# Optimization experiments

Hardware: AMD Instinct MI355X
Metric: run time of the kernel (lower is better)

Reference implementation:

```python
import jax, jax.numpy as jnp
import numpy as np

B, NQ, NKV = 2, 1024, 4096
DQ = 1024          # query_dim == context_dim
H, DH = 16, 64     # heads, dim_head
INNER = H * DH     # 1024
SCALE = DH ** -0.5


def setup_inputs() -> dict:
    key = jax.random.key(0)
    ks = jax.random.split(key, 6)
    s = 1.0 / np.sqrt(DQ)
    return {
        "x": jax.random.normal(ks[0], (B, NQ, DQ), dtype=jnp.float32),
        "context": jax.random.normal(ks[1], (B, NKV, DQ), dtype=jnp.float32),
        "Wq": jax.random.normal(ks[2], (DQ, INNER), dtype=jnp.float32) * s,
        "Wkv": jax.random.normal(ks[3], (DQ, 2 * INNER), dtype=jnp.float32) * s,
        "Wout": jax.random.normal(ks[4], (INNER, DQ), dtype=jnp.float32) * (1.0 / np.sqrt(INNER)),
        "b_out": jax.random.normal(ks[5], (DQ,), dtype=jnp.float32) * 0.01,
    }


def _split_heads(t):
    # b n (h d) -> b h n d
    b, n, _ = t.shape
    return t.reshape(b, n, H, DH).transpose(0, 2, 1, 3)


def reference(x, context, Wq, Wkv, Wout, b_out):
    q = x @ Wq                       # [B, NQ, INNER]
    kv = context @ Wkv               # [B, NKV, 2*INNER]
    k, v = jnp.split(kv, 2, axis=-1)
    q, k, v = map(_split_heads, (q, k, v))          # [B, H, n, DH]
    sim = jnp.einsum("bhid,bhjd->bhij", q, k) * SCALE  # [B, H, NQ, NKV]
    attn = jax.nn.softmax(sim, axis=-1)
    out = jnp.einsum("bhij,bhjd->bhid", attn, v)       # [B, H, NQ, DH]
    out = out.transpose(0, 2, 1, 3).reshape(B, NQ, INNER)  # (b h) n d -> b n (h d)
    return out @ Wout + b_out
```

## Files before the change

### kernel.cpp

```cpp
#include <hip/hip_runtime.h>
#include <stdint.h>

#define B_    2
#define NQ_   1024
#define NKV_  4096
#define DQ_   1024
#define H_    16
#define DH_   64
#define INNER_ 1024

typedef unsigned short u16;
typedef uint32_t u32;
typedef __bf16 bf16x8 __attribute__((ext_vector_type(8)));
typedef float  f32x4  __attribute__((ext_vector_type(4)));

__device__ __forceinline__ u16 f2bf(float x) {
  union { float f; uint32_t u; } v; v.f = x;
  uint32_t r = v.u + 0x7FFFu + ((v.u >> 16) & 1u);
  return (u16)(r >> 16);
}
__device__ __forceinline__ u32 pack2(float a, float b) {
  return (u32)f2bf(a) | ((u32)f2bf(b) << 16);
}
__device__ __forceinline__ u32 pack2rn(float a, float b) {
  union { float f; u32 u; } x, y; x.f = a; y.f = b;
  return __builtin_amdgcn_perm(y.u + 0x8000u, x.u + 0x8000u, 0x07060302u);
}
__device__ __forceinline__ float bf2f(u16 s) {
  union { float f; uint32_t u; } v; v.u = ((uint32_t)s) << 16; return v.f;
}

__device__ __forceinline__ void gload16(const void* g, void* l) {
  __builtin_amdgcn_global_load_lds((const __attribute__((address_space(1))) void*)g,
                                   (__attribute__((address_space(3))) void*)l,
                                   16, 0, 0);
}

__global__ __launch_bounds__(256) void prep(const float* __restrict__ x,
                                            const float* __restrict__ ctx,
                                            const float* __restrict__ Wq,
                                            const float* __restrict__ Wkv,
                                            const float* __restrict__ Wout,
                                            u16* __restrict__ xb,
                                            u16* __restrict__ ctxb,
                                            u16* __restrict__ WqT,
                                            u16* __restrict__ WkvT,
                                            u16* __restrict__ WoutT) {
  int bid = blockIdx.x;
  if (bid < 1280) {
    const float* src; u16* dst; int fbase;
    if (bid < 256) { src = x;   dst = xb;   fbase = bid * 2048; }
    else           { src = ctx; dst = ctxb; fbase = (bid - 256) * 2048; }
#pragma unroll
    for (int u = 0; u < 8; ++u) {
      int i = (fbase + u * 256 + threadIdx.x) * 4;
      float4 v = *(const float4*)(src + i);
      uint2 o; o.x = pack2(v.x, v.y); o.y = pack2(v.z, v.w);
      *(uint2*)(dst + i) = o;
    }
    return;
  }
  __shared__ float tile[32][33];
  const float* W; u16* Wt; int K, N, local, nsh;
  int b2 = bid - 1280;
  if (b2 < 1024)      { W = Wq;   Wt = WqT;   K = 1024; N = 1024; local = b2;        nsh = 5; }
  else if (b2 < 3072) { W = Wkv;  Wt = WkvT;  K = 1024; N = 2048; local = b2 - 1024; nsh = 6; }
  else                { W = Wout; Wt = WoutT; K = 1024; N = 1024; local = b2 - 3072; nsh = 5; }
  int n0 = (local & ((1 << nsh) - 1)) * 32;
  int k0 = (local >> nsh) * 32;
  int tx = threadIdx.x & 31, ty = threadIdx.x >> 5;
  for (int i = ty; i < 32; i += 8)
    tile[i][tx] = W[(size_t)(k0 + i) * N + n0 + tx];
  __syncthreads();
  for (int i = ty; i < 32; i += 8)
    Wt[(size_t)(n0 + i) * K + k0 + tx] = f2bf(tile[tx][i]);
}

__global__ __launch_bounds__(512, 2) void kv_gemm(const u16* __restrict__ ctxb,
                                                  const u16* __restrict__ WkvT,
                                                  u16* __restrict__ kb,
                                                  u16* __restrict__ vTb) {
  __shared__ __align__(16) u16 As[2][256 * 64];
  __shared__ __align__(16) u16 Bs[2][256 * 64];
  const int tid = threadIdx.x;
  const int lane = tid & 63;
  const int w = tid >> 6;
  const int wr = w >> 2, wc = w & 3;
  const int l15 = lane & 15, quad = lane >> 4;
  const int K = 1024;

  int bid = blockIdx.x;
  int wgid = (bid & 7) * 32 + (bid >> 3);
  const int tm = wgid >> 3, tn = wgid & 7;
  const int m0 = tm * 256, n0 = tn * 256;
  const u16* Ag = ctxb + (size_t)m0 * K;
  const u16* Bg = WkvT + (size_t)n0 * K;

  size_t offA[2][2], offB[2][2];
#pragma unroll
  for (int ah = 0; ah < 2; ++ah)
#pragma unroll
    for (int p = 0; p < 2; ++p) {
      int c = p * 512 + (w << 6) + lane;
      int s = ah * 128 + (c >> 3);
      int col = ((c & 7) ^ (s & 7)) << 3;
      int rA = ((s >> 6) & 1) * 128 + ((s >> 7) & 1) * 64 + (s & 63);
      int rB = ((s >> 5) & 3) * 64 + ((s >> 7) & 1) * 32 + (s & 31);
      offA[ah][p] = (size_t)rA * 1024 + col;
      offB[ah][p] = (size_t)rB * 1024 + col;
    }

#define STAGE_A(bufi, ah, kk) do { \
    gload16(Ag + offA[ah][0] + (kk), &As[bufi][(ah) * 8192 + (w << 9)]); \
    gload16(Ag + offA[ah][1] + (kk), &As[bufi][(ah) * 8192 + 4096 + (w << 9)]); \
  } while (0)
#define STAGE_B(bufi, bh, kk) do { \
    gload16(Bg + offB[bh][0] + (kk), &Bs[bufi][(bh) * 8192 + (w << 9)]); \
    gload16(Bg + offB[bh][1] + (kk), &Bs[bufi][(bh) * 8192 + 4096 + (w << 9)]); \
  } while (0)
#define LDA2(dst, i8, bufi) do { \
    const int _s = ((i8) >> 2) * 128 + wr * 64 + ((i8) & 3) * 16 + l15; \
    const u16* _p = &As[bufi][_s * 64]; const int _x = _s & 7; \
    dst[0] = *(const bf16x8*)&_p[(quad ^ _x) << 3]; \
    dst[1] = *(const bf16x8*)&_p[((quad + 4) ^ _x) << 3]; \
  } while (0)
#define LDB2(dst, j, bufi) do { \
    const int _s = ((j) >> 1) * 128 + wc * 32 + ((j) & 1) * 16 + l15; \
    const u16* _p = &Bs[bufi][_s * 64]; const int _x = _s & 7; \
    dst[0] = *(const bf16x8*)&_p[(quad ^ _x) << 3]; \
    dst[1] = *(const bf16x8*)&_p[((quad + 4) ^ _x) << 3]; \
  } while (0)
#define MF(i0, j0, bb) do { \
    _Pragma("unroll") \
    for (int _i = 0; _i < 4; ++_i) { \
      acc[(i0) + _i][(j0)    ] = __builtin_amdgcn_mfma_f32_16x16x32_bf16(a[_i][0], bb[0][0], acc[(i0) + _i][(j0)    ], 0, 0, 0); \
      acc[(i0) + _i][(j0)    ] = __builtin_amdgcn_mfma_f32_16x16x32_bf16(a[_i][1], bb[0][1], acc[(i0) + _i][(j0)    ], 0, 0, 0); \
      acc[(i0) + _i][(j0) + 1] = __builtin_amdgcn_mfma_f32_16x16x32_bf16(a[_i][0], bb[1][0], acc[(i0) + _i][(j0) + 1], 0, 0, 0); \
      acc[(i0) + _i][(j0) + 1] = __builtin_amdgcn_mfma_f32_16x16x32_bf16(a[_i][1], bb[1][1], acc[(i0) + _i][(j0) + 1], 0, 0, 0); \
    } \
  } while (0)

  f32x4 acc[8][4] = {};
  bf16x8 a[4][2], b[2][2], c2[2][2];

  STAGE_A(0, 0, 0);
  STAGE_B(0, 0, 0);
  STAGE_B(0, 1, 0);
  STAGE_A(0, 1, 0);
  asm volatile("s_waitcnt vmcnt(4)" ::: "memory");
  __builtin_amdgcn_s_barrier();

#define KTILE(cur, nxt, kk, STG, W1, W2) do { \
     \
    LDB2(b[0], 0, cur); LDB2(b[1], 1, cur); \
    LDA2(a[0], 0, cur); LDA2(a[1], 1, cur); LDA2(a[2], 2, cur); LDA2(a[3], 3, cur); \
    if (STG) STAGE_A(nxt, 0, kk); \
    __builtin_amdgcn_s_barrier(); \
    asm volatile("s_waitcnt lgkmcnt(0)" ::: "memory"); \
    __builtin_amdgcn_s_setprio(1); MF(0, 0, b); __builtin_amdgcn_s_setprio(0); \
    asm volatile("s_waitcnt " W1 ::: "memory"); \
    __builtin_amdgcn_s_barrier(); \
     \
    LDB2(c2[0], 2, cur); LDB2(c2[1], 3, cur); \
    if (STG) STAGE_B(nxt, 0, kk); \
    __builtin_amdgcn_s_barrier(); \
    asm volatile("s_waitcnt lgkmcnt(0)" ::: "memory"); \
    __builtin_amdgcn_s_setprio(1); MF(0, 2, c2); __builtin_amdgcn_s_setprio(0); \
    asm volatile("s_waitcnt " W2 ::: "memory"); \
    __builtin_amdgcn_s_barrier(); \
     \
    LDA2(a[0], 4, cur); LDA2(a[1], 5, cur); LDA2(a[2], 6, cur); LDA2(a[3], 7, cur); \
    if (STG) STAGE_B(nxt, 1, kk); \
    __builtin_amdgcn_s_barrier(); \
    asm volatile("s_waitcnt lgkmcnt(0)" ::: "memory"); \
    __builtin_amdgcn_s_setprio(1); MF(4, 0, b); __builtin_amdgcn_s_setprio(0); \
    __builtin_amdgcn_s_barrier(); \
     \
    if (STG) STAGE_A(nxt, 1, kk); \
    __builtin_amdgcn_s_barrier(); \
    __builtin_amdgcn_s_setprio(1); MF(4, 2, c2); __builtin_amdgcn_s_setprio(0); \
    if (STG) { asm volatile("s_waitcnt vmcnt(4)" ::: "memory"); } \
    __builtin_amdgcn_s_barrier(); \
  } while (0)

  for (int T = 0; T < 15; ++T) {
    const int cur = T & 1, nxt = cur ^ 1, kk = (T + 1) * 64;
    KTILE(cur, nxt, kk, 1, "vmcnt(4)", "vmcnt(4)");
  }
  KTILE(1, 0, 0, 0, "vmcnt(2)", "vmcnt(0)");

  if (tn < 4) {
#pragma unroll
    for (int i8 = 0; i8 < 8; ++i8)
#pragma unroll
      for (int j = 0; j < 4; ++j) {
        int col = n0 + wc * 64 + j * 16 + l15;
#pragma unroll
        for (int r = 0; r < 4; ++r) {
          int row = m0 + wr * 128 + i8 * 16 + quad * 4 + r;
          kb[(size_t)row * 1024 + col] = f2bf(acc[i8][j][r]);
        }
      }
  } else {
    const int bb_ = m0 >> 12;
#pragma unroll
    for (int i8 = 0; i8 < 8; ++i8) {
      int kvr = (m0 & 4095) + wr * 128 + i8 * 16 + quad * 4;
#pragma unroll
      for (int j = 0; j < 4; ++j) {
        int c = (n0 - 1024) + wc * 64 + j * 16 + l15;
        int h = c >> 6, dh = c & 63;
        uint2 st;
        st.x = pack2(acc[i8][j][0], acc[i8][j][1]);
        st.y = pack2(acc[i8][j][2], acc[i8][j][3]);
        *(uint2*)&vTb[((size_t)((bb_ * 16 + h) * 64 + dh)) * NKV_ + kvr] = st;
      }
    }
  }
#undef STAGE_A
#undef STAGE_B
#undef LDA2
#undef LDB2
#undef MF
#undef KTILE
}

__global__ __launch_bounds__(256) void q_gemm(const u16* __restrict__ A,
                                              const u16* __restrict__ Bt,
                                              u16* __restrict__ outp) {
  __shared__ __align__(16) u16 As[64 * 32];
  __shared__ __align__(16) u16 Bs[128 * 32];
  const int tid = threadIdx.x;
  const int lane = tid & 63;
  const int w = tid >> 6;
  const int wr = w >> 1, wc = w & 1;
  const int l15 = lane & 15, quad = lane >> 4;
  const int unit = blockIdx.x;
  const int m0 = (unit >> 3) * 64, n0 = (unit & 7) * 128;
  const int K = 1024, N = 1024;

  const u16* Ab = A + (size_t)m0 * K;
  const u16* Bb = Bt + (size_t)n0 * K;
  f32x4 acc[2][4] = {};

  const int ar = tid >> 2, ac = (tid & 3) << 3;
  const int q1 = w * 64 + lane, q2 = q1 + 256;
  const int br1 = q1 >> 2, bc1 = (q1 & 3) << 3;
  const int br2 = q2 >> 2, bc2 = (q2 & 3) << 3;

  for (int k0 = 0; k0 < K; k0 += 32) {
    __syncthreads();
    gload16(Ab + (size_t)ar * K + k0 + ac, &As[w * 512]);
    gload16(Bb + (size_t)br1 * K + k0 + bc1, &Bs[w * 512]);
    gload16(Bb + (size_t)br2 * K + k0 + bc2, &Bs[2048 + w * 512]);
    __syncthreads();
    bf16x8 af[2], bfr[4];
#pragma unroll
    for (int i = 0; i < 2; ++i)
      af[i] = *(const bf16x8*)&As[(wr * 32 + i * 16 + l15) * 32 + quad * 8];
#pragma unroll
    for (int j = 0; j < 4; ++j)
      bfr[j] = *(const bf16x8*)&Bs[(wc * 64 + j * 16 + l15) * 32 + quad * 8];
#pragma unroll
    for (int i = 0; i < 2; ++i)
#pragma unroll
      for (int j = 0; j < 4; ++j)
        acc[i][j] = __builtin_amdgcn_mfma_f32_16x16x32_bf16(af[i], bfr[j], acc[i][j], 0, 0, 0);
  }

#pragma unroll
  for (int i = 0; i < 2; ++i)
#pragma unroll
    for (int j = 0; j < 4; ++j) {
      int col = n0 + wc * 64 + j * 16 + l15;
#pragma unroll
      for (int r = 0; r < 4; ++r) {
        int row = m0 + wr * 32 + i * 16 + quad * 4 + r;
        outp[(size_t)row * N + col] = f2bf(acc[i][j][r]);
      }
    }
}

__global__ __launch_bounds__(256) void out_gemm(const u16* __restrict__ A,
                                                const u16* __restrict__ Bt,
                                                float* __restrict__ Cout,
                                                const float* __restrict__ bias) {
  __shared__ __align__(16) u16 As[64 * 32];
  __shared__ __align__(16) u16 Bs[128 * 32];
  const int tid = threadIdx.x;
  const int lane = tid & 63;
  const int w = tid >> 6;
  const int wr = w >> 1, wc = w & 1;
  const int l15 = lane & 15, quad = lane >> 4;
  const int unit = blockIdx.x;
  const int m0 = (unit >> 3) * 64, n0 = (unit & 7) * 128;
  const int K = 1024, N = 1024;

  const u16* Ab = A + (size_t)m0 * K;
  const u16* Bb = Bt + (size_t)n0 * K;
  f32x4 acc[2][4] = {};

  const int ar = tid >> 2, ac = (tid & 3) << 3;
  const int q1 = w * 64 + lane, q2 = q1 + 256;
  const int br1 = q1 >> 2, bc1 = (q1 & 3) << 3;
  const int br2 = q2 >> 2, bc2 = (q2 & 3) << 3;

  for (int k0 = 0; k0 < K; k0 += 32) {
    __syncthreads();
    gload16(Ab + (size_t)ar * K + k0 + ac, &As[w * 512]);
    gload16(Bb + (size_t)br1 * K + k0 + bc1, &Bs[w * 512]);
    gload16(Bb + (size_t)br2 * K + k0 + bc2, &Bs[2048 + w * 512]);
    __syncthreads();
    bf16x8 af[2], bfr[4];
#pragma unroll
    for (int i = 0; i < 2; ++i)
      af[i] = *(const bf16x8*)&As[(wr * 32 + i * 16 + l15) * 32 + quad * 8];
#pragma unroll
    for (int j = 0; j < 4; ++j)
      bfr[j] = *(const bf16x8*)&Bs[(wc * 64 + j * 16 + l15) * 32 + quad * 8];
#pragma unroll
    for (int i = 0; i < 2; ++i)
#pragma unroll
      for (int j = 0; j < 4; ++j)
        acc[i][j] = __builtin_amdgcn_mfma_f32_16x16x32_bf16(af[i], bfr[j], acc[i][j], 0, 0, 0);
  }

#pragma unroll
  for (int i = 0; i < 2; ++i)
#pragma unroll
    for (int j = 0; j < 4; ++j) {
      int col = n0 + wc * 64 + j * 16 + l15;
      float bv = bias[col];
#pragma unroll
      for (int r = 0; r < 4; ++r) {
        int row = m0 + wr * 32 + i * 16 + quad * 4 + r;
        Cout[(size_t)row * N + col] = acc[i][j][r] + bv;
      }
    }
}

__global__ __launch_bounds__(256, 2) void attn_kernel(const u16* __restrict__ qg,
                                                      const u16* __restrict__ kb,
                                                      const u16* __restrict__ vT,
                                                      u16* __restrict__ attn_out) {
  __shared__ __align__(16) u16 Ks[128 * 64];
  __shared__ __align__(16) u16 Vs[64 * 128];
  __shared__ __align__(16) u32 P32[4 * 4 * 16 * 20];
  __shared__ float Lr[4][4][16];

  const int tid = threadIdx.x;
  const int lane = tid & 63;
  const int w = tid >> 6;
  const int l15 = lane & 15, quad = lane >> 4;
  const int bh = blockIdx.x, b = bh >> 4, h = bh & 15;
  const int q0 = blockIdx.y * 64;

  const float SC = 0.125f * 1.44269504088896340736f;
  union { u16 s[8]; bf16x8 v; } qf[4][2];
#pragma unroll
  for (int t = 0; t < 4; ++t)
#pragma unroll
    for (int kc = 0; kc < 2; ++kc) {
      const u16* qp = qg + (size_t)(b * NQ_ + q0 + t * 16 + l15) * INNER_ + h * 64 +
                      kc * 32 + quad * 8;
      union { u16 s[8]; uint4 u; } tmp;
      tmp.u = *(const uint4*)qp;
#pragma unroll
      for (int e = 0; e < 8; ++e) qf[t][kc].s[e] = f2bf(bf2f(tmp.s[e]) * SC);
    }

#define STAGEKV(j0) do { \
    _Pragma("unroll") \
    for (int i_ = 0; i_ < 4; ++i_) { \
      int s_ = i_ * 256 + tid; \
      int kr = s_ >> 3, kg = (s_ ^ kr) & 7; \
      gload16(kb + (size_t)(b * NKV_ + (j0) + kr) * 1024 + h * 64 + kg * 8, \
              &Ks[(i_ * 256 + w * 64) * 8]); \
      int vr = s_ >> 4, vg = (s_ ^ vr) & 15; \
      gload16(vT + (size_t)(bh * 64 + vr) * NKV_ + (j0) + vg * 8, \
              &Vs[(i_ * 256 + w * 64) * 8]); \
    } \
  } while (0)

  f32x4 Oacc[4][4] = {};
  float l_lane[4] = {0.f, 0.f, 0.f, 0.f};

  STAGEKV(0);

  for (int it = 0; it < 32; ++it) {
    __syncthreads();

    bf16x8 kf[2][2];
#pragma unroll
    for (int kvt = 0; kvt < 2; ++kvt)
#pragma unroll
      for (int kc = 0; kc < 2; ++kc)
        kf[kvt][kc] = *(const bf16x8*)
          &Ks[(w * 32 + kvt * 16 + l15) * 64 + (((kc * 4 + quad) ^ l15) & 7) * 8];
    bf16x8 vf[4];
#pragma unroll
    for (int d = 0; d < 4; ++d)
      vf[d] = *(const bf16x8*)
        &Vs[(d * 16 + l15) * 128 + (((w * 4 + quad) ^ l15) & 15) * 8];

    __syncthreads();

    if (it < 31) STAGEKV((it + 1) * 128);

    f32x4 sacc[2][4] = {};
    __builtin_amdgcn_s_setprio(1);
#pragma unroll
    for (int kvt = 0; kvt < 2; ++kvt)
#pragma unroll
      for (int t = 0; t < 4; ++t)
#pragma unroll
        for (int kc = 0; kc < 2; ++kc)
          sacc[kvt][t] = __builtin_amdgcn_mfma_f32_16x16x32_bf16(
              kf[kvt][kc], qf[t][kc].v, sacc[kvt][t], 0, 0, 0);
    __builtin_amdgcn_s_setprio(0);

#pragma unroll
    for (int kvt = 0; kvt < 2; ++kvt)
#pragma unroll
      for (int t = 0; t < 4; ++t) {
        float p0 = __builtin_amdgcn_exp2f(sacc[kvt][t][0]);
        float p1 = __builtin_amdgcn_exp2f(sacc[kvt][t][1]);
        float p2 = __builtin_amdgcn_exp2f(sacc[kvt][t][2]);
        float p3 = __builtin_amdgcn_exp2f(sacc[kvt][t][3]);
        l_lane[t] += (p0 + p1) + (p2 + p3);
        uint2 pk; pk.x = pack2rn(p0, p1); pk.y = pack2rn(p2, p3);
        *(uint2*)&P32[((w * 4 + t) * 16 + l15) * 20 + kvt * 8 + quad * 2] = pk;
      }

    bf16x8 pf[4];
#pragma unroll
    for (int t = 0; t < 4; ++t)
      pf[t] = *(const bf16x8*)&P32[((w * 4 + t) * 16 + l15) * 20 + quad * 4];
    __builtin_amdgcn_s_setprio(1);
#pragma unroll
    for (int d = 0; d < 4; ++d)
#pragma unroll
      for (int t = 0; t < 4; ++t)
        Oacc[d][t] = __builtin_amdgcn_mfma_f32_16x16x32_bf16(vf[d], pf[t], Oacc[d][t],
                                                             0, 0, 0);
    __builtin_amdgcn_s_setprio(0);
  }
#undef STAGEKV

#pragma unroll
  for (int t = 0; t < 4; ++t) {
    l_lane[t] += __shfl_xor(l_lane[t], 16);
    l_lane[t] += __shfl_xor(l_lane[t], 32);
  }
  if (quad == 0) {
#pragma unroll
    for (int t = 0; t < 4; ++t) Lr[w][t][l15] = l_lane[t];
  }
  __syncthreads();
  float inv = 1.0f / (Lr[0][w][l15] + Lr[1][w][l15] + Lr[2][w][l15] + Lr[3][w][l15]);

  float* red = (float*)P32;
  u16* ob = attn_out + (size_t)(b * NQ_ + q0 + w * 16 + l15) * INNER_ + h * 64;
#pragma unroll
  for (int d = 0; d < 4; ++d) {
    __syncthreads();
#pragma unroll
    for (int t = 0; t < 4; ++t)
      *(f32x4*)&red[(w * 4 + t) * 256 + quad * 64 + l15 * 4] = Oacc[d][t];
    __syncthreads();
    f32x4 r = *(const f32x4*)&red[(0 * 4 + w) * 256 + quad * 64 + l15 * 4];
#pragma unroll
    for (int ww = 1; ww < 4; ++ww) {
      f32x4 c = *(const f32x4*)&red[(ww * 4 + w) * 256 + quad * 64 + l15 * 4];
      r[0] += c[0]; r[1] += c[1]; r[2] += c[2]; r[3] += c[3];
    }
    *(u32*)(ob + d * 16 + quad * 4)     = pack2(r[0] * inv, r[1] * inv);
    *(u32*)(ob + d * 16 + quad * 4 + 2) = pack2(r[2] * inv, r[3] * inv);
  }
}

extern "C" void kernel_launch(void* const* d_in, const int* in_sizes, int n_in,
                              void* d_out, int out_size, void* d_ws, size_t ws_size,
                              hipStream_t stream) {
  const float* x    = (const float*)d_in[0];
  const float* ctx  = (const float*)d_in[1];
  const float* Wq   = (const float*)d_in[2];
  const float* Wkv  = (const float*)d_in[3];
  const float* Wout = (const float*)d_in[4];
  const float* bout = (const float*)d_in[5];

  char* ws = (char*)d_ws;
  u16* xb    = (u16*)(ws + (size_t)( 0u << 20));
  u16* ab    = (u16*)(ws + (size_t)( 0u << 20));
  u16* ctxb  = (u16*)(ws + (size_t)( 4u << 20));
  u16* WqT   = (u16*)(ws + (size_t)(20u << 20));
  u16* WkvT  = (u16*)(ws + (size_t)(22u << 20));
  u16* WoutT = (u16*)(ws + (size_t)(26u << 20));
  u16* qb    = (u16*)(ws + (size_t)(28u << 20));
  u16* kb    = (u16*)(ws + (size_t)(32u << 20));
  u16* vTb   = (u16*)(ws + (size_t)(48u << 20));

  prep<<<5376, 256, 0, stream>>>(x, ctx, Wq, Wkv, Wout, xb, ctxb, WqT, WkvT, WoutT);
  q_gemm<<<256, 256, 0, stream>>>(xb, WqT, qb);
  kv_gemm<<<256, 512, 0, stream>>>(ctxb, WkvT, kb, vTb);
  attn_kernel<<<dim3(32, 16), 256, 0, stream>>>(qb, kb, vTb, ab);
  out_gemm<<<256, 256, 0, stream>>>(ab, WoutT, (float*)d_out, bout);
}
```

Before: 228.5 us.

## Pre-tile K/V into per-wave images, drop block barriers and LDS P round-trip

The KV GEMM epilogue now writes K and V^T in a tiled, pre-swizzled per-(bh, 128-row tile, wave) layout. Each attention wave can then stage its own contiguous 32-key slice into a private double-buffered LDS region with no __syncthreads in the main loop. The softmax probabilities are packed with v_cvt_pk_bf16_f32 and rearranged into the PV MFMA operand layout using permlane32_swap and shuffles, replacing the write-then-read through LDS. This removes block-wide barriers and LDS traffic in the hot loop, at the cost of more cross-lane ops and a more scattered epilogue store pattern in the projection GEMM.

```diff
diff --git a/kernel.cpp b/kernel.cpp
--- a/kernel.cpp
+++ b/kernel.cpp
@@ -22,9 +22,10 @@
 __device__ __forceinline__ u32 pack2(float a, float b) {
   return (u32)f2bf(a) | ((u32)f2bf(b) << 16);
 }
-__device__ __forceinline__ u32 pack2rn(float a, float b) {
-  union { float f; u32 u; } x, y; x.f = a; y.f = b;
-  return __builtin_amdgcn_perm(y.u + 0x8000u, x.u + 0x8000u, 0x07060302u);
+__device__ __forceinline__ u32 cvtpk(float lo, float hi) {
+  u32 r;
+  asm("v_cvt_pk_bf16_f32 %0, %1, %2" : "=v"(r) : "v"(lo), "v"(hi));
+  return r;
 }
 __device__ __forceinline__ float bf2f(u16 s) {
   union { float f; uint32_t u; } v; v.u = ((uint32_t)s) << 16; return v.f;
@@ -151,7 +152,6 @@
   __builtin_amdgcn_s_barrier();
 
 #define KTILE(cur, nxt, kk, STG, W1, W2) do { \
-     \
     LDB2(b[0], 0, cur); LDB2(b[1], 1, cur); \
     LDA2(a[0], 0, cur); LDA2(a[1], 1, cur); LDA2(a[2], 2, cur); LDA2(a[3], 3, cur); \
     if (STG) STAGE_A(nxt, 0, kk); \
@@ -160,7 +160,6 @@
     __builtin_amdgcn_s_setprio(1); MF(0, 0, b); __builtin_amdgcn_s_setprio(0); \
     asm volatile("s_waitcnt " W1 ::: "memory"); \
     __builtin_amdgcn_s_barrier(); \
-     \
     LDB2(c2[0], 2, cur); LDB2(c2[1], 3, cur); \
     if (STG) STAGE_B(nxt, 0, kk); \
     __builtin_amdgcn_s_barrier(); \
@@ -168,14 +167,12 @@
     __builtin_amdgcn_s_setprio(1); MF(0, 2, c2); __builtin_amdgcn_s_setprio(0); \
     asm volatile("s_waitcnt " W2 ::: "memory"); \
     __builtin_amdgcn_s_barrier(); \
-     \
     LDA2(a[0], 4, cur); LDA2(a[1], 5, cur); LDA2(a[2], 6, cur); LDA2(a[3], 7, cur); \
     if (STG) STAGE_B(nxt, 1, kk); \
     __builtin_amdgcn_s_barrier(); \
     asm volatile("s_waitcnt lgkmcnt(0)" ::: "memory"); \
     __builtin_amdgcn_s_setprio(1); MF(4, 0, b); __builtin_amdgcn_s_setprio(0); \
     __builtin_amdgcn_s_barrier(); \
-     \
     if (STG) STAGE_A(nxt, 1, kk); \
     __builtin_amdgcn_s_barrier(); \
     __builtin_amdgcn_s_setprio(1); MF(4, 2, c2); __builtin_amdgcn_s_setprio(0); \
@@ -190,30 +187,38 @@
   KTILE(1, 0, 0, 0, "vmcnt(2)", "vmcnt(0)");
 
   if (tn < 4) {
-#pragma unroll
-    for (int i8 = 0; i8 < 8; ++i8)
+    const int b_ = m0 >> 12;
+    const int h_ = (n0 >> 6) + wc;
+    const int bh_ = b_ * 16 + h_;
+    const int it0 = ((m0 & 4095) >> 7) + wr;
+    const int e = l15 & 7;
+#pragma unroll
+    for (int i8 = 0; i8 < 8; ++i8) {
+      const size_t reg_ = ((size_t)(bh_ * 32 + it0) * 4 + (i8 >> 1)) * 2048;
 #pragma unroll
       for (int j = 0; j < 4; ++j) {
-        int col = n0 + wc * 64 + j * 16 + l15;
+        const int gd = j * 2 + (l15 >> 3);
 #pragma unroll
         for (int r = 0; r < 4; ++r) {
-          int row = m0 + wr * 128 + i8 * 16 + quad * 4 + r;
-          kb[(size_t)row * 1024 + col] = f2bf(acc[i8][j][r]);
+          const int rl = (i8 & 1) * 16 + quad * 4 + r;
+          kb[reg_ + rl * 64 + ((gd ^ rl) & 7) * 8 + e] = f2bf(acc[i8][j][r]);
         }
       }
+    }
   } else {
-    const int bb_ = m0 >> 12;
+    const int b_ = m0 >> 12;
+    const int h_ = ((n0 - 1024) >> 6) + wc;
+    const int bh_ = b_ * 16 + h_;
+    const int it0 = ((m0 & 4095) >> 7) + wr;
 #pragma unroll
     for (int i8 = 0; i8 < 8; ++i8) {
-      int kvr = (m0 & 4095) + wr * 128 + i8 * 16 + quad * 4;
+      const size_t reg_ = ((size_t)(bh_ * 32 + it0) * 4 + (i8 >> 1)) * 2048;
 #pragma unroll
       for (int j = 0; j < 4; ++j) {
-        int c = (n0 - 1024) + wc * 64 + j * 16 + l15;
-        int h = c >> 6, dh = c & 63;
         uint2 st;
         st.x = pack2(acc[i8][j][0], acc[i8][j][1]);
         st.y = pack2(acc[i8][j][2], acc[i8][j][3]);
-        *(uint2*)&vTb[((size_t)((bb_ * 16 + h) * 64 + dh)) * NKV_ + kvr] = st;
+        *(uint2*)&vTb[reg_ + (size_t)(j * 16 + l15) * 32 + (i8 & 1) * 16 + quad * 4] = st;
       }
     }
   }
@@ -339,15 +344,14 @@
     }
 }
 
-__global__ __launch_bounds__(256, 2) void attn_kernel(const u16* __restrict__ qg,
-                                                      const u16* __restrict__ kb,
-                                                      const u16* __restrict__ vT,
+__global__ __launch_bounds__(256, 2) void attn_kernel(const u16* __restrict__ kimg_q,
+                                                      const u16* __restrict__ kimg,
+                                                      const u16* __restrict__ vimg,
                                                       u16* __restrict__ attn_out) {
-  __shared__ __align__(16) u16 Ks[128 * 64];
-  __shared__ __align__(16) u16 Vs[64 * 128];
-  __shared__ __align__(16) u32 P32[4 * 4 * 16 * 20];
+  __shared__ __align__(16) u16 KV[4][2][4096];
   __shared__ float Lr[4][4][16];
 
+  const u16* qg = kimg_q;
   const int tid = threadIdx.x;
   const int lane = tid & 63;
   const int w = tid >> 6;
@@ -369,73 +373,88 @@
       for (int e = 0; e < 8; ++e) qf[t][kc].s[e] = f2bf(bf2f(tmp.s[e]) * SC);
     }
 
-#define STAGEKV(j0) do { \
-    _Pragma("unroll") \
-    for (int i_ = 0; i_ < 4; ++i_) { \
-      int s_ = i_ * 256 + tid; \
-      int kr = s_ >> 3, kg = (s_ ^ kr) & 7; \
-      gload16(kb + (size_t)(b * NKV_ + (j0) + kr) * 1024 + h * 64 + kg * 8, \
-              &Ks[(i_ * 256 + w * 64) * 8]); \
-      int vr = s_ >> 4, vg = (s_ ^ vr) & 15; \
-      gload16(vT + (size_t)(bh * 64 + vr) * NKV_ + (j0) + vg * 8, \
-              &Vs[(i_ * 256 + w * 64) * 8]); \
-    } \
+  const u16* kg = kimg + ((size_t)(bh * 32) * 4 + w) * 2048 + lane * 8;
+  const u16* vg = vimg + ((size_t)(bh * 32) * 4 + w) * 2048 + lane * 8;
+
+#define STAGE(bf, itv) do { \
+    const size_t _o = (size_t)(itv) * 8192; \
+    gload16(kg + _o,        &KV[w][bf][0]); \
+    gload16(kg + _o + 512,  &KV[w][bf][512]); \
+    gload16(kg + _o + 1024, &KV[w][bf][1024]); \
+    gload16(kg + _o + 1536, &KV[w][bf][1536]); \
+    gload16(vg + _o,        &KV[w][bf][2048]); \
+    gload16(vg + _o + 512,  &KV[w][bf][2560]); \
+    gload16(vg + _o + 1024, &KV[w][bf][3072]); \
+    gload16(vg + _o + 1536, &KV[w][bf][3584]); \
   } while (0)
 
   f32x4 Oacc[4][4] = {};
   float l_lane[4] = {0.f, 0.f, 0.f, 0.f};
 
-  STAGEKV(0);
+  STAGE(0, 0);
 
   for (int it = 0; it < 32; ++it) {
-    __syncthreads();
-
-    bf16x8 kf[2][2];
+    const int bf = it & 1;
+    if (it < 31) {
+      STAGE(bf ^ 1, it + 1);
+      asm volatile("s_waitcnt vmcnt(8)" ::: "memory");
+    } else {
+      asm volatile("s_waitcnt vmcnt(0)" ::: "memory");
+    }
+
+    bf16x8 kf[2][2], vf[4];
 #pragma unroll
     for (int kvt = 0; kvt < 2; ++kvt)
 #pragma unroll
       for (int kc = 0; kc < 2; ++kc)
         kf[kvt][kc] = *(const bf16x8*)
-          &Ks[(w * 32 + kvt * 16 + l15) * 64 + (((kc * 4 + quad) ^ l15) & 7) * 8];
-    bf16x8 vf[4];
+          &KV[w][bf][(kvt * 16 + l15) * 64 + (((kc * 4 + quad) ^ l15) & 7) * 8];
 #pragma unroll
     for (int d = 0; d < 4; ++d)
-      vf[d] = *(const bf16x8*)
-        &Vs[(d * 16 + l15) * 128 + (((w * 4 + quad) ^ l15) & 15) * 8];
-
-    __syncthreads();
-
-    if (it < 31) STAGEKV((it + 1) * 128);
+      vf[d] = *(const bf16x8*)&KV[w][bf][2048 + (d * 16 + l15) * 32 + quad * 8];
 
     f32x4 sacc[2][4] = {};
     __builtin_amdgcn_s_setprio(1);
 #pragma unroll
     for (int kvt = 0; kvt < 2; ++kvt)
 #pragma unroll
-      for (int t = 0; t < 4; ++t)
-#pragma unroll
-        for (int kc = 0; kc < 2; ++kc)
-          sacc[kvt][t] = __builtin_amdgcn_mfma_f32_16x16x32_bf16(
-              kf[kvt][kc], qf[t][kc].v, sacc[kvt][t], 0, 0, 0);
+      for (int t = 0; t < 4; ++t) {
+        sacc[kvt][t] = __builtin_amdgcn_mfma_f32_16x16x32_bf16(
+            kf[kvt][0], qf[t][0].v, sacc[kvt][t], 0, 0, 0);
+        sacc[kvt][t] = __builtin_amdgcn_mfma_f32_16x16x32_bf16(
+            kf[kvt][1], qf[t][1].v, sacc[kvt][t], 0, 0, 0);
+      }
     __builtin_amdgcn_s_setprio(0);
 
-#pragma unroll
-    for (int kvt = 0; kvt < 2; ++kvt)
-#pragma unroll
-      for (int t = 0; t < 4; ++t) {
-        float p0 = __builtin_amdgcn_exp2f(sacc[kvt][t][0]);
-        float p1 = __builtin_amdgcn_exp2f(sacc[kvt][t][1]);
-        float p2 = __builtin_amdgcn_exp2f(sacc[kvt][t][2]);
-        float p3 = __builtin_amdgcn_exp2f(sacc[kvt][t][3]);
-        l_lane[t] += (p0 + p1) + (p2 + p3);
-        uint2 pk; pk.x = pack2rn(p0, p1); pk.y = pack2rn(p2, p3);
-        *(uint2*)&P32[((w * 4 + t) * 16 + l15) * 20 + kvt * 8 + quad * 2] = pk;
-      }
-
     bf16x8 pf[4];
 #pragma unroll
-    for (int t = 0; t < 4; ++t)
-      pf[t] = *(const bf16x8*)&P32[((w * 4 + t) * 16 + l15) * 20 + quad * 4];
+    for (int t = 0; t < 4; ++t) {
+      float p0 = __builtin_amdgcn_exp2f(sacc[0][t][0]);
+      float p1 = __builtin_amdgcn_exp2f(sacc[0][t][1]);
+      float p2 = __builtin_amdgcn_exp2f(sacc[0][t][2]);
+      float p3 = __builtin_amdgcn_exp2f(sacc[0][t][3]);
+      float p4 = __builtin_amdgcn_exp2f(sacc[1][t][0]);
+      float p5 = __builtin_amdgcn_exp2f(sacc[1][t][1]);
+      float p6 = __builtin_amdgcn_exp2f(sacc[1][t][2]);
+      float p7 = __builtin_amdgcn_exp2f(sacc[1][t][3]);
+      l_lane[t] += ((p0 + p1) + (p2 + p3)) + ((p4 + p5) + (p6 + p7));
+      u32 A0 = cvtpk(p0, p1), A1 = cvtpk(p2, p3);
+      u32 B0 = cvtpk(p4, p5), B1 = cvtpk(p6, p7);
+      asm("v_permlane32_swap_b32 %0, %1" : "+v"(A0), "+v"(B0));
+      asm("v_permlane32_swap_b32 %0, %1" : "+v"(A1), "+v"(B1));
+      u32 sx16 = (u32)__shfl_xor((int)A0, 16);
+      u32 sy16 = (u32)__shfl_xor((int)B0, 16);
+      u32 tx16 = (u32)__shfl_xor((int)A1, 16);
+      u32 ty16 = (u32)__shfl_xor((int)B1, 16);
+      const bool odd = (quad & 1);
+      union { u32 u[4]; bf16x8 v; } pk_;
+      pk_.u[0] = odd ? sy16 : A0;
+      pk_.u[1] = odd ? ty16 : A1;
+      pk_.u[2] = odd ? B0   : sx16;
+      pk_.u[3] = odd ? B1   : tx16;
+      pf[t] = pk_.v;
+    }
+
     __builtin_amdgcn_s_setprio(1);
 #pragma unroll
     for (int d = 0; d < 4; ++d)
@@ -445,7 +464,7 @@
                                                              0, 0, 0);
     __builtin_amdgcn_s_setprio(0);
   }
-#undef STAGEKV
+#undef STAGE
 
 #pragma unroll
   for (int t = 0; t < 4; ++t) {
@@ -459,7 +478,7 @@
   __syncthreads();
   float inv = 1.0f / (Lr[0][w][l15] + Lr[1][w][l15] + Lr[2][w][l15] + Lr[3][w][l15]);
 
-  float* red = (float*)P32;
+  float* red = (float*)&KV[0][0][0];
   u16* ob = attn_out + (size_t)(b * NQ_ + q0 + w * 16 + l15) * INNER_ + h * 64;
 #pragma unroll
   for (int d = 0; d < 4; ++d) {
```

New measurement: 226.5 us. No clear change (-0.9%).

## Deepen KV GEMM prefetch pipeline by staggering global-to-LDS staging across buffers

Applied to the files above, without the earlier changes.

Restructures the KV projection GEMM main loop so that staging for the next-next K tile is issued into the buffer just consumed. A-half staging is interleaved one tile ahead, and more loads stay in flight (vmcnt(6) instead of vmcnt(4)). The per-phase vmcnt waits between barriers are removed, leaving a single wait per half-tile. The goal is to hide more global-memory latency behind MFMA work, at the cost of more complex buffer-hazard reasoning, where a mis-ordered wait could read stale LDS data.

```diff
diff --git a/kernel.cpp b/kernel.cpp
--- a/kernel.cpp
+++ b/kernel.cpp
@@ -139,6 +139,8 @@
       acc[(i0) + _i][(j0) + 1] = __builtin_amdgcn_mfma_f32_16x16x32_bf16(a[_i][1], bb[1][1], acc[(i0) + _i][(j0) + 1], 0, 0, 0); \
     } \
   } while (0)
+#define BAR()   __builtin_amdgcn_s_barrier()
+#define LGKM0() asm volatile("s_waitcnt lgkmcnt(0)" ::: "memory")
 
   f32x4 acc[8][4] = {};
   bf16x8 a[4][2], b[2][2], c2[2][2];
@@ -147,47 +149,54 @@
   STAGE_B(0, 0, 0);
   STAGE_B(0, 1, 0);
   STAGE_A(0, 1, 0);
-  asm volatile("s_waitcnt vmcnt(4)" ::: "memory");
-  __builtin_amdgcn_s_barrier();
-
-#define KTILE(cur, nxt, kk, STG, W1, W2) do { \
+  STAGE_A(1, 0, 64);
+  STAGE_B(1, 0, 64);
+  STAGE_B(1, 1, 64);
+  asm volatile("s_waitcnt vmcnt(6)" ::: "memory");
+  BAR();
+
+#define HALF(bufi, kAb, kNext, STG, WMID, WEND) do { \
      \
-    LDB2(b[0], 0, cur); LDB2(b[1], 1, cur); \
-    LDA2(a[0], 0, cur); LDA2(a[1], 1, cur); LDA2(a[2], 2, cur); LDA2(a[3], 3, cur); \
-    if (STG) STAGE_A(nxt, 0, kk); \
-    __builtin_amdgcn_s_barrier(); \
-    asm volatile("s_waitcnt lgkmcnt(0)" ::: "memory"); \
+    LDB2(b[0], 0, bufi); LDB2(b[1], 1, bufi); \
+    LDA2(a[0], 0, bufi); LDA2(a[1], 1, bufi); LDA2(a[2], 2, bufi); LDA2(a[3], 3, bufi); \
+    if (kAb >= 0) STAGE_A((bufi) ^ 1, 1, kAb); \
+    BAR(); LGKM0(); \
     __builtin_amdgcn_s_setprio(1); MF(0, 0, b); __builtin_amdgcn_s_setprio(0); \
-    asm volatile("s_waitcnt " W1 ::: "memory"); \
-    __builtin_amdgcn_s_barrier(); \
+    BAR(); \
      \
-    LDB2(c2[0], 2, cur); LDB2(c2[1], 3, cur); \
-    if (STG) STAGE_B(nxt, 0, kk); \
-    __builtin_amdgcn_s_barrier(); \
-    asm volatile("s_waitcnt lgkmcnt(0)" ::: "memory"); \
+    LDB2(c2[0], 2, bufi); LDB2(c2[1], 3, bufi); \
+    if (STG) STAGE_A(bufi, 0, kNext); \
+    BAR(); LGKM0(); \
     __builtin_amdgcn_s_setprio(1); MF(0, 2, c2); __builtin_amdgcn_s_setprio(0); \
-    asm volatile("s_waitcnt " W2 ::: "memory"); \
-    __builtin_amdgcn_s_barrier(); \
+    BAR(); \
      \
-    LDA2(a[0], 4, cur); LDA2(a[1], 5, cur); LDA2(a[2], 6, cur); LDA2(a[3], 7, cur); \
-    if (STG) STAGE_B(nxt, 1, kk); \
-    __builtin_amdgcn_s_barrier(); \
-    asm volatile("s_waitcnt lgkmcnt(0)" ::: "memory"); \
+    LDA2(a[0], 4, bufi); LDA2(a[1], 5, bufi); LDA2(a[2], 6, bufi); LDA2(a[3], 7, bufi); \
+    if (STG) STAGE_B(bufi, 0, kNext); \
+    BAR(); LGKM0(); \
     __builtin_amdgcn_s_setprio(1); MF(4, 0, b); __builtin_amdgcn_s_setprio(0); \
-    __builtin_amdgcn_s_barrier(); \
+    BAR(); \
      \
-    if (STG) STAGE_A(nxt, 1, kk); \
-    __builtin_amdgcn_s_barrier(); \
+    if (STG) STAGE_B(bufi, 1, kNext); \
+    BAR(); \
     __builtin_amdgcn_s_setprio(1); MF(4, 2, c2); __builtin_amdgcn_s_setprio(0); \
-    if (STG) { asm volatile("s_waitcnt vmcnt(4)" ::: "memory"); } \
-    __builtin_amdgcn_s_barrier(); \
-  } while (0)
-
-  for (int T = 0; T < 15; ++T) {
-    const int cur = T & 1, nxt = cur ^ 1, kk = (T + 1) * 64;
-    KTILE(cur, nxt, kk, 1, "vmcnt(4)", "vmcnt(4)");
-  }
-  KTILE(1, 0, 0, 0, "vmcnt(2)", "vmcnt(0)");
+    WMID; \
+    BAR(); \
+  } while (0)
+
+  for (int i = 0; i < 7; ++i) {
+    const int k2 = i * 128;
+    HALF(0, k2 + 64, k2 + 128, 1,
+         asm volatile("s_waitcnt vmcnt(6)" ::: "memory"), );
+    HALF(1, k2 + 128, k2 + 192, 1,
+         asm volatile("s_waitcnt vmcnt(6)" ::: "memory"), );
+  }
+  HALF(0, 960, 0, 0,
+       asm volatile("s_waitcnt vmcnt(0)" ::: "memory"), );
+  HALF(1, -1, 0, 0, , );
+
+#undef HALF
+#undef BAR
+#undef LGKM0
 
   if (tn < 4) {
 #pragma unroll
@@ -222,7 +231,6 @@
 #undef LDA2
 #undef LDB2
 #undef MF
-#undef KTILE
 }
 
 __global__ __launch_bounds__(256) void q_gemm(const u16* __restrict__ A,
```

Result: faster. 221.5 us (-3.1%).
